# Optimization experiments

Measured on AMD Instinct MI355X. Metric: run time of the kernel, lower is better.

## Reference

```python
import jax, jax.numpy as jnp
import numpy as np

NUM_CLASSES = 7000
FEAT_DIM = 128
N = 524288
ALPHA = 0.5


def setup_inputs() -> dict:
    key = jax.random.key(0)
    k1, k2, k3 = jax.random.split(key, 3)
    features = jax.random.normal(k1, (N, FEAT_DIM), dtype=jnp.float32)
    labels = jax.random.randint(k2, (N,), 0, NUM_CLASSES, dtype=jnp.int32)
    centers = jax.random.normal(k3, (NUM_CLASSES, FEAT_DIM), dtype=jnp.float32)
    return {"features": features, "labels": labels, "centers": centers}


def reference(features, labels, centers):
    """Center loss: gather centers, l2 loss, count-scaled scatter-sub update.

    Mirrors get_center_loss:
      centers_batch = tf.gather(centers, labels)
      loss = tf.nn.l2_loss(features - centers_batch)  # 0.5 * sum(sq)
      appear_times = per-sample count of its label (unique_with_counts + gather)
      diff = alpha * (centers_batch - features) / (1 + appear_times)
      centers <- scatter_sub(centers, labels, diff)
    Returns (loss, updated_centers).
    """
    num_classes = centers.shape[0]
    centers_batch = centers[labels]                       # [N, D] gather
    delta = features - centers_batch                      # [N, D]
    loss = 0.5 * jnp.sum(delta * delta)                   # tf.nn.l2_loss

    # unique_with_counts -> gather(count, idx) == per-row occurrence count
    counts = jax.ops.segment_sum(
        jnp.ones_like(labels, dtype=jnp.float32), labels,
        num_segments=num_classes)                         # [C]
    appear_times = counts[labels]                         # [N]

    scale = ALPHA / (1.0 + appear_times)                  # [N]
    diff = -delta * scale[:, None]                        # centers_batch - features, scaled
    new_centers = centers.at[labels].add(-diff)           # scatter_sub
    return loss, new_centers
```

## Files before the change

### kernel.cpp

```cpp
#include <hip/hip_runtime.h>

#define NUM_CLASSES 7000
#define FEAT_DIM    128
#define NSAMP       524288
#define ALPHA       0.5f
#define MAXN        256

__global__ void scatter_k(const int* __restrict__ labels,
                          int* __restrict__ cursors,
                          int* __restrict__ order) {
    int i = blockIdx.x * blockDim.x + threadIdx.x;
    if (i < NSAMP) {
        int c = labels[i];
        int pos = atomicAdd(&cursors[c], 1);
        if (pos < MAXN) order[(c << 8) + pos] = i;
    }
}

__launch_bounds__(256)
__global__ void update_k(const float* __restrict__ features,
                         const float* __restrict__ centers,
                         const int* __restrict__ cursors,
                         const int* __restrict__ order,
                         float* __restrict__ out_loss,
                         float* __restrict__ new_centers)
{
    const int c    = blockIdx.x;
    const int tid  = threadIdx.x;
    const int ul   = tid & 31;
    const int unit = tid >> 5;
    const int wave = tid >> 6;
    const int lane = tid & 63;

    const int n    = min(cursors[c], MAXN);
    const int base = c << 8;

    const float4* __restrict__ f4 = (const float4*)features;
    const float4* __restrict__ c4 = (const float4*)centers;
    const float4 cen = c4[c * 32 + ul];

    float ax = 0.f, ay = 0.f, az = 0.f, aw = 0.f, lacc = 0.f;

    int k = unit;
    if (k < n) {
        int i = order[base + k];
        for (;;) {
            const int k2 = k + 8;
            int inext = 0;
            if (k2 < n) inext = order[base + k2];
            const float4 f = f4[i * 32 + ul];
            const float dx = f.x - cen.x;
            const float dy = f.y - cen.y;
            const float dz = f.z - cen.z;
            const float dw = f.w - cen.w;
            ax += dx; ay += dy; az += dz; aw += dw;
            lacc += dx * dx + dy * dy + dz * dz + dw * dw;
            if (k2 >= n) break;
            k = k2; i = inext;
        }
    }

    __shared__ float red[8][FEAT_DIM];
    __shared__ float lred[4];
    red[unit][4 * ul + 0] = ax;
    red[unit][4 * ul + 1] = ay;
    red[unit][4 * ul + 2] = az;
    red[unit][4 * ul + 3] = aw;
    for (int off = 32; off; off >>= 1) lacc += __shfl_down(lacc, off, 64);
    if (lane == 0) lred[wave] = lacc;
    __syncthreads();

    if (tid < FEAT_DIM) {
        const float s = red[0][tid] + red[1][tid] + red[2][tid] + red[3][tid]
                      + red[4][tid] + red[5][tid] + red[6][tid] + red[7][tid];
        const float scale = ALPHA / (1.0f + (float)n);
        new_centers[c * FEAT_DIM + tid] = centers[c * FEAT_DIM + tid] + scale * s;
    }
    if (tid == 0)
        atomicAdd(out_loss, 0.5f * (lred[0] + lred[1] + lred[2] + lred[3]));
}

extern "C" void kernel_launch(void* const* d_in, const int* in_sizes, int n_in,
                              void* d_out, int out_size, void* d_ws, size_t ws_size,
                              hipStream_t stream) {
    const float* features = (const float*)d_in[0];
    const int*   labels   = (const int*)d_in[1];
    const float* centers  = (const float*)d_in[2];

    int* cursors = (int*)d_ws;
    int* order   = cursors + NUM_CLASSES;

    float* out_loss    = (float*)d_out;
    float* out_centers = out_loss + 1;

    hipMemsetAsync(cursors, 0, NUM_CLASSES * sizeof(int), stream);
    hipMemsetAsync(out_loss, 0, sizeof(float), stream);

    scatter_k<<<(NSAMP + 255) / 256, 256, 0, stream>>>(labels, cursors, order);
    update_k<<<NUM_CLASSES, 256, 0, stream>>>(features, centers, cursors, order,
                                              out_loss, out_centers);
}
```

Before: 423.0 us.

## Unroll gathered feature loads, vectorize label scatter, replace memsets with zero kernel

The update kernel now gives each 32-lane unit a contiguous chunk of sample indices. It loads those indices once into lanes, broadcasts them with shuffles, and issues four independent feature row loads per iteration, so more memory requests are in flight. The scatter kernel reads labels as int4 and does four atomics per thread, and the two memsets become one small zeroing kernel. The LDS store of partial sums is also vectorized. This adds register pressure and relies on chunk sizes of at most 32 (n≤256 split across 8 units), and atomic contention in the scatter is unchanged.

```diff
diff --git a/kernel.cpp b/kernel.cpp
--- a/kernel.cpp
+++ b/kernel.cpp
@@ -6,14 +6,24 @@
 #define ALPHA       0.5f
 #define MAXN        256
 
+__global__ void zero_k(int* __restrict__ cursors, float* __restrict__ out_loss) {
+    int i = blockIdx.x * blockDim.x + threadIdx.x;
+    if (i < NUM_CLASSES) cursors[i] = 0;
+    if (i == 0) out_loss[0] = 0.0f;
+}
+
 __global__ void scatter_k(const int* __restrict__ labels,
                           int* __restrict__ cursors,
                           int* __restrict__ order) {
-    int i = blockIdx.x * blockDim.x + threadIdx.x;
-    if (i < NSAMP) {
-        int c = labels[i];
-        int pos = atomicAdd(&cursors[c], 1);
-        if (pos < MAXN) order[(c << 8) + pos] = i;
+    int t = blockIdx.x * blockDim.x + threadIdx.x;
+    int i0 = t << 2;
+    if (i0 < NSAMP) {
+        const int4 lab = ((const int4*)labels)[t];
+        int c, p;
+        c = lab.x; p = atomicAdd(&cursors[c], 1); if (p < MAXN) order[(c << 8) + p] = i0;
+        c = lab.y; p = atomicAdd(&cursors[c], 1); if (p < MAXN) order[(c << 8) + p] = i0 + 1;
+        c = lab.z; p = atomicAdd(&cursors[c], 1); if (p < MAXN) order[(c << 8) + p] = i0 + 2;
+        c = lab.w; p = atomicAdd(&cursors[c], 1); if (p < MAXN) order[(c << 8) + p] = i0 + 3;
     }
 }
 
@@ -35,37 +45,49 @@
     const int n    = min(cursors[c], MAXN);
     const int base = c << 8;
 
+    const int chunk = (n + 7) >> 3;
+    const int rbeg  = unit * chunk;
+    const int m     = min(chunk, n - rbeg) > 0 ? min(chunk, n - rbeg) : 0;
+
+    int myidx = 0;
+    if (ul < m) myidx = order[base + rbeg + ul];
+
     const float4* __restrict__ f4 = (const float4*)features;
-    const float4* __restrict__ c4 = (const float4*)centers;
-    const float4 cen = c4[c * 32 + ul];
+    const float4 cen = ((const float4*)centers)[c * 32 + ul];
 
     float ax = 0.f, ay = 0.f, az = 0.f, aw = 0.f, lacc = 0.f;
 
-    int k = unit;
-    if (k < n) {
-        int i = order[base + k];
-        for (;;) {
-            const int k2 = k + 8;
-            int inext = 0;
-            if (k2 < n) inext = order[base + k2];
-            const float4 f = f4[i * 32 + ul];
-            const float dx = f.x - cen.x;
-            const float dy = f.y - cen.y;
-            const float dz = f.z - cen.z;
-            const float dw = f.w - cen.w;
-            ax += dx; ay += dy; az += dz; aw += dw;
-            lacc += dx * dx + dy * dy + dz * dz + dw * dw;
-            if (k2 >= n) break;
-            k = k2; i = inext;
-        }
+    int j = 0;
+    for (; j + 4 <= m; j += 4) {
+        const int i0 = __shfl(myidx, j,     32);
+        const int i1 = __shfl(myidx, j + 1, 32);
+        const int i2 = __shfl(myidx, j + 2, 32);
+        const int i3 = __shfl(myidx, j + 3, 32);
+        const float4 f0 = f4[i0 * 32 + ul];
+        const float4 f1 = f4[i1 * 32 + ul];
+        const float4 f2 = f4[i2 * 32 + ul];
+        const float4 f3 = f4[i3 * 32 + ul];
+        float dx, dy, dz, dw;
+        dx = f0.x - cen.x; dy = f0.y - cen.y; dz = f0.z - cen.z; dw = f0.w - cen.w;
+        ax += dx; ay += dy; az += dz; aw += dw; lacc += dx*dx + dy*dy + dz*dz + dw*dw;
+        dx = f1.x - cen.x; dy = f1.y - cen.y; dz = f1.z - cen.z; dw = f1.w - cen.w;
+        ax += dx; ay += dy; az += dz; aw += dw; lacc += dx*dx + dy*dy + dz*dz + dw*dw;
+        dx = f2.x - cen.x; dy = f2.y - cen.y; dz = f2.z - cen.z; dw = f2.w - cen.w;
+        ax += dx; ay += dy; az += dz; aw += dw; lacc += dx*dx + dy*dy + dz*dz + dw*dw;
+        dx = f3.x - cen.x; dy = f3.y - cen.y; dz = f3.z - cen.z; dw = f3.w - cen.w;
+        ax += dx; ay += dy; az += dz; aw += dw; lacc += dx*dx + dy*dy + dz*dz + dw*dw;
+    }
+    for (; j < m; ++j) {
+        const int i0 = __shfl(myidx, j, 32);
+        const float4 f0 = f4[i0 * 32 + ul];
+        float dx, dy, dz, dw;
+        dx = f0.x - cen.x; dy = f0.y - cen.y; dz = f0.z - cen.z; dw = f0.w - cen.w;
+        ax += dx; ay += dy; az += dz; aw += dw; lacc += dx*dx + dy*dy + dz*dz + dw*dw;
     }
 
     __shared__ float red[8][FEAT_DIM];
     __shared__ float lred[4];
-    red[unit][4 * ul + 0] = ax;
-    red[unit][4 * ul + 1] = ay;
-    red[unit][4 * ul + 2] = az;
-    red[unit][4 * ul + 3] = aw;
+    ((float4*)red[unit])[ul] = make_float4(ax, ay, az, aw);
     for (int off = 32; off; off >>= 1) lacc += __shfl_down(lacc, off, 64);
     if (lane == 0) lred[wave] = lacc;
     __syncthreads();
@@ -93,10 +115,8 @@
     float* out_loss    = (float*)d_out;
     float* out_centers = out_loss + 1;
 
-    hipMemsetAsync(cursors, 0, NUM_CLASSES * sizeof(int), stream);
-    hipMemsetAsync(out_loss, 0, sizeof(float), stream);
-
-    scatter_k<<<(NSAMP + 255) / 256, 256, 0, stream>>>(labels, cursors, order);
+    zero_k<<<(NUM_CLASSES + 255) / 256, 256, 0, stream>>>(cursors, out_loss);
+    scatter_k<<<(NSAMP / 4 + 255) / 256, 256, 0, stream>>>(labels, cursors, order);
     update_k<<<NUM_CLASSES, 256, 0, stream>>>(features, centers, cursors, order,
                                               out_loss, out_centers);
 }
```

New measurement: 410.8 us. 2.9% less time.
